# Optimization experiments

Hardware: AMD Instinct MI355X
Metric: run time of the kernel (lower is better)

Reference implementation:

```python
import jax, jax.numpy as jnp
import numpy as np

N = 30000      # num_nodes
R0 = 8         # original relations
R = 2 * R0 + 1 # with inverses + self-loop relation = 17
IN = 256
OUT = 256
E = 300000     # original triples
NB = 8         # num_bases


def setup_inputs() -> dict:
    key = jax.random.key(0)
    k1, k2, k3, k4, k5, k6 = jax.random.split(key, 6)
    s = jax.random.randint(k1, (E,), 0, N)
    r = jax.random.randint(k2, (E,), 0, R0)
    o = jax.random.randint(k3, (E,), 0, N)
    triples = jnp.stack([s, r, o], axis=1)  # [E,3] int
    features = jax.random.normal(k4, (N, IN), dtype=jnp.float32)
    bases = jax.random.normal(k5, (NB, IN, OUT), dtype=jnp.float32) * 0.02
    comps = jax.random.normal(k6, (R, NB), dtype=jnp.float32) * 0.02
    bias = jnp.zeros((OUT,), dtype=jnp.float32)
    return {"triples": triples, "features": features, "bases": bases, "comps": comps, "bias": bias}


def reference(triples, features, bases, comps, bias):
    # basis decomposition: weights[r] = sum_b comps[r,b] * bases[b]
    weights = jnp.einsum('rb,bio->rio', comps, bases)  # [R, IN, OUT]

    s, r, o = triples[:, 0], triples[:, 1], triples[:, 2]
    nodes = jnp.arange(N)
    # eval mode: self_loop_keep_prob = 1 -> all N self loops kept
    src = jnp.concatenate([s, o, nodes])                                  # [E + E + N]
    rel = jnp.concatenate([r, r + R0, jnp.full((N,), 2 * R0, r.dtype)])
    dst = jnp.concatenate([o, s, nodes])

    # horizontal stacking: adj is [N, R*N]; row = src, col = rel*N + dst
    cols = rel * N + dst
    # column normalisation (row_normalisation=False branch of sum_sparse)
    col_sums = jnp.zeros((R * N,), jnp.float32).at[cols].add(1.0)
    sums = col_sums[cols]
    # reorder: swap normalizers of original and inverse edge blocks
    sums = jnp.concatenate([sums[E:2 * E], sums[:E], sums[2 * E:]])
    vals = 1.0 / sums

    # fw[r*N + n] = features[n] @ weights[r]
    fw = jnp.einsum('ni,rio->rno', features, weights).reshape(R * N, OUT)
    msgs = vals[:, None] * fw[cols]                    # [num_edges, OUT]
    out = jnp.zeros((N, OUT), jnp.float32).at[src].add(msgs)
    return out + bias
```

## Files before the change

kernel.cpp:

```cpp
#include <hip/hip_runtime.h>


namespace {
constexpr int kN     = 30000;
constexpr int kR0    = 8;
constexpr int kNRel  = 16;
constexpr int kIN    = 256;
constexpr int kOUT   = 256;
constexpr int kE     = 300000;
constexpr int kNB    = 8;
constexpr int kKT    = kNB * kIN;
constexpr int kRows  = kN * kNRel;
constexpr int kMsgs  = 2 * kE;
constexpr int kScanBlk  = 1024;
constexpr int kNScanBlk = (kRows + kScanBlk - 1) / kScanBlk;
constexpr int kBM    = 128;
constexpr int kMB    = (kN + kBM - 1) / kBM;
constexpr int kMPadAlloc = 30016;
constexpr int kTN    = 16;
}

typedef __bf16 bf16x8 __attribute__((ext_vector_type(8)));
typedef float  f32x4  __attribute__((ext_vector_type(4)));
typedef float  f32x2  __attribute__((ext_vector_type(2)));
typedef float  f32x4v __attribute__((ext_vector_type(4)));
typedef unsigned int u32;

static __device__ __forceinline__ ushort f2bf(float x) {
  unsigned u = __float_as_uint(x);
  u += 0x7FFF + ((u >> 16) & 1);
  return (ushort)(u >> 16);
}

static __device__ __forceinline__ void gload16(const void* g, void* l) {
  __builtin_amdgcn_global_load_lds(
      (const __attribute__((address_space(1))) u32*)g,
      (__attribute__((address_space(3))) u32*)l, 16, 0, 0);
}

#define PKFMA_LO(ACC, G, C) \
  asm("v_pk_fma_f32 %0, %1, %2, %0 op_sel_hi:[1,0,1]" : "+v"(ACC) : "v"(G), "v"(C))
#define PKFMA_HI(ACC, G, C) \
  asm("v_pk_fma_f32 %0, %1, %2, %0 op_sel:[0,1,0] op_sel_hi:[1,1,1]" : "+v"(ACC) : "v"(G), "v"(C))


__global__ void k_prep(const float* __restrict__ f, ushort* __restrict__ fb,
                       const int* __restrict__ t, int* __restrict__ deg,
                       const float* __restrict__ bases, ushort* __restrict__ Bt) {
  int i = blockIdx.x * 256 + threadIdx.x;
  if (i < kN * kIN / 4) {
    float4 v = reinterpret_cast<const float4*>(f)[i];
    ushort4 p;
    p.x = f2bf(v.x); p.y = f2bf(v.y); p.z = f2bf(v.z); p.w = f2bf(v.w);
    reinterpret_cast<ushort4*>(fb)[i] = p;
  }
  if (i < kE) {
    int s = t[3*i], r = t[3*i+1], o = t[3*i+2];
    atomicAdd(&deg[s * kNRel + r], 1);
    atomicAdd(&deg[o * kNRel + kR0 + r], 1);
  }
  if (blockIdx.x < kKT / 16) {
    int b  = blockIdx.x;
    int tt = threadIdx.x;
    char* dst = (char*)Bt + (size_t)tt * 4096;
    int xr = (tt & 7) << 4;
#pragma unroll
    for (int q = 0; q < 4; ++q) {
      int k0 = b * 16 + q * 4;
      ushort4 p;
      p.x = f2bf(bases[(size_t)(k0 + 0) * kOUT + tt]);
      p.y = f2bf(bases[(size_t)(k0 + 1) * kOUT + tt]);
      p.z = f2bf(bases[(size_t)(k0 + 2) * kOUT + tt]);
      p.w = f2bf(bases[(size_t)(k0 + 3) * kOUT + tt]);
      *reinterpret_cast<ushort4*>(dst + ((b * 32 + q * 8) ^ xr)) = p;
    }
  }
}


__global__ void k_scan1(const int* __restrict__ deg, int* __restrict__ rp,
                        int* __restrict__ blksum) {
  __shared__ int s[256];
  int tid = threadIdx.x;
  int base = blockIdx.x * kScanBlk + tid * 4;
  int v0 = 0, v1 = 0, v2 = 0, v3 = 0;
  if (base + 3 < kRows) {
    v0 = deg[base]; v1 = deg[base+1]; v2 = deg[base+2]; v3 = deg[base+3];
  } else {
    if (base     < kRows) v0 = deg[base];
    if (base + 1 < kRows) v1 = deg[base+1];
    if (base + 2 < kRows) v2 = deg[base+2];
  }
  int t0 = v0, t1 = t0 + v1, t2 = t1 + v2, t3 = t2 + v3;
  s[tid] = t3;
  __syncthreads();
  for (int off = 1; off < 256; off <<= 1) {
    int x = 0;
    if (tid >= off) x = s[tid - off];
    __syncthreads();
    s[tid] += x;
    __syncthreads();
  }
  int excl = tid ? s[tid-1] : 0;
  if (base     < kRows) rp[base]   = excl;
  if (base + 1 < kRows) rp[base+1] = excl + t0;
  if (base + 2 < kRows) rp[base+2] = excl + t1;
  if (base + 3 < kRows) rp[base+3] = excl + t2;
  if (tid == 255) blksum[blockIdx.x] = s[255];
}

__global__ void k_scan3(int* __restrict__ rp, const int* __restrict__ blksum) {
  __shared__ int red[256];
  int tid = threadIdx.x;
  int B   = blockIdx.x;
  int region = (B * 256) >> 10;
  int partial = 0;
  for (int k = tid; k < region; k += 256) partial += blksum[k];
  red[tid] = partial;
  __syncthreads();
#pragma unroll
  for (int off = 128; off > 0; off >>= 1) {
    if (tid < off) red[tid] += red[tid + off];
    __syncthreads();
  }
  int base = red[0];
  int i = B * 256 + tid;
  if (i < kRows)       rp[i] += base;
  else if (i == kRows) rp[i]  = kMsgs;
}

__global__ void k_scatter(const int* __restrict__ t, const int* __restrict__ rp,
                          int* __restrict__ deg, int* __restrict__ col) {
  int m = blockIdx.x * 256 + threadIdx.x;
  if (m >= kMsgs) return;
  int e = (m < kE) ? m : m - kE;
  int s = t[3*e], r = t[3*e+1], o = t[3*e+2];
  int rr, tn, sn;
  if (m < kE) { rr = r;        tn = s; sn = o; }
  else        { rr = kR0 + r;  tn = o; sn = s; }
  int idx = tn * kNRel + rr;
  int pos = rp[idx] + (atomicSub(&deg[idx], 1) - 1);
  col[pos] = (rr << 16) | sn;
}

#define FMA4(A, S, G) \
  A.x += (S) * G.x; A.y += (S) * G.y; A.z += (S) * G.z; A.w += (S) * G.w;


__global__ __launch_bounds__(256, 8)
void k_agg1(const int* __restrict__ rp, const int* __restrict__ col,
            const ushort* __restrict__ featbf, const float* __restrict__ comps,
            ushort* __restrict__ aggb) {
  __shared__ float cvb[4][17][kNB];
  int wv   = threadIdx.x >> 6;
  int lane = threadIdx.x & 63;
  int node = blockIdx.x * 4 + wv;

  if (lane < 17) {
    float val = 0.f;
    if (lane < kNRel) {
      int idx = node * kNRel + lane;
      int d = rp[idx + 1] - rp[idx];
      val = d > 0 ? 1.0f / (float)d : 0.f;
    }
#pragma unroll
    for (int b = 0; b < kNB; ++b)
      cvb[wv][lane][b] = comps[lane * kNB + b] * val;
  }
  __syncthreads();

  int se0 = __builtin_amdgcn_readfirstlane(rp[node * kNRel]);
  int se1 = __builtin_amdgcn_readfirstlane(rp[node * kNRel + kNRel]);

  f32x2 accp[2 * kNB];
  {
    uint2 sf = *reinterpret_cast<const uint2*>(featbf + (size_t)node * kIN + lane * 4);
    f32x2 p01, p23;
    p01.x = __uint_as_float(sf.x << 16);
    p01.y = __uint_as_float(sf.x & 0xFFFF0000u);
    p23.x = __uint_as_float(sf.y << 16);
    p23.y = __uint_as_float(sf.y & 0xFFFF0000u);
#pragma unroll
    for (int b = 0; b < kNB; ++b) {
      float cs = comps[2*kR0*kNB + b];
      accp[2*b]     = p01 * cs;
      accp[2*b + 1] = p23 * cs;
    }
  }

  const int pad = (16 << 16);
  int voff = lane * 4;
  const f32x4v* cvr = reinterpret_cast<const f32x4v*>(&cvb[wv][0][0]);

  auto compute = [&](const uint2* g, const int* sc) {
#pragma unroll
    for (int j = 0; j < 4; ++j) {
      int sr = sc[j] >> 16;
      f32x4v cA = cvr[sr * 2];
      f32x4v cB = cvr[sr * 2 + 1];
      f32x2 p01, p23;
      p01.x = __uint_as_float(g[j].x << 16);
      p01.y = __uint_as_float(g[j].x & 0xFFFF0000u);
      p23.x = __uint_as_float(g[j].y << 16);
      p23.y = __uint_as_float(g[j].y & 0xFFFF0000u);
      f32x2 cAl = cA.lo, cAh = cA.hi, cBl = cB.lo, cBh = cB.hi;
      PKFMA_LO(accp[0],  p01, cAl); PKFMA_LO(accp[1],  p23, cAl);
      PKFMA_HI(accp[2],  p01, cAl); PKFMA_HI(accp[3],  p23, cAl);
      PKFMA_LO(accp[4],  p01, cAh); PKFMA_LO(accp[5],  p23, cAh);
      PKFMA_HI(accp[6],  p01, cAh); PKFMA_HI(accp[7],  p23, cAh);
      PKFMA_LO(accp[8],  p01, cBl); PKFMA_LO(accp[9],  p23, cBl);
      PKFMA_HI(accp[10], p01, cBl); PKFMA_HI(accp[11], p23, cBl);
      PKFMA_LO(accp[12], p01, cBh); PKFMA_LO(accp[13], p23, cBh);
      PKFMA_HI(accp[14], p01, cBh); PKFMA_HI(accp[15], p23, cBh);
    }
  };

  int sc0[4], sc1[4];
  uint2 g0[4];
#pragma unroll
  for (int j = 0; j < 4; ++j) {
    int ee = se0 + j;
    int ic = ee < se1 ? ee : 0;
    int v  = col[ic];
    sc0[j] = ee < se1 ? v : pad;
  }
#pragma unroll
  for (int j = 0; j < 4; ++j)
    g0[j] = *reinterpret_cast<const uint2*>(featbf + (size_t)(sc0[j] & 0xFFFF) * kIN + voff);
#pragma unroll
  for (int j = 0; j < 4; ++j) {
    int ee = se0 + 4 + j;
    int ic = ee < se1 ? ee : 0;
    int v  = col[ic];
    sc1[j] = ee < se1 ? v : pad;
  }

  for (int e = se0; e + 4 < se1; e += 4) {
    uint2 g1[4];
#pragma unroll
    for (int j = 0; j < 4; ++j)
      g1[j] = *reinterpret_cast<const uint2*>(featbf + (size_t)(sc1[j] & 0xFFFF) * kIN + voff);
    int sc2[4];
#pragma unroll
    for (int j = 0; j < 4; ++j) {
      int ee = e + 8 + j;
      int ic = ee < se1 ? ee : 0;
      int v  = col[ic];
      sc2[j] = ee < se1 ? v : pad;
    }
    compute(g0, sc0);
#pragma unroll
    for (int j = 0; j < 4; ++j) { g0[j] = g1[j]; sc0[j] = sc1[j]; sc1[j] = sc2[j]; }
  }
  if (se0 < se1) compute(g0, sc0);

  char* rowp = (char*)aggb + (size_t)node * 4096;
  int xr = (node & 7) << 4;
#pragma unroll
  for (int b = 0; b < kNB; ++b) {
    ushort4 p;
    p.x = f2bf(accp[2*b].x);     p.y = f2bf(accp[2*b].y);
    p.z = f2bf(accp[2*b + 1].x); p.w = f2bf(accp[2*b + 1].y);
    *reinterpret_cast<ushort4*>(rowp + ((b * 512 + lane * 8) ^ xr)) = p;
  }
}


__global__ __launch_bounds__(1024, 4)
void k_gemm(const ushort* __restrict__ aggb, const ushort* __restrict__ Bt,
            const float* __restrict__ bias, float* __restrict__ out) {
  __shared__ ushort Albs[2][kBM * 64];
  __shared__ ushort Blds[2][256 * 64];
  int tid  = threadIdx.x;
  int wv   = tid >> 6;
  int lane = tid & 63;
  int mh   = wv >> 2;
  int nq   = wv & 3;
  int l15  = lane & 15;
  int g4   = lane >> 4;
  int node0 = blockIdx.x * kBM;

  f32x4 acc[2][4];
#pragma unroll
  for (int mt = 0; mt < 2; ++mt)
#pragma unroll
    for (int nt = 0; nt < 4; ++nt) acc[mt][nt] = f32x4{0.f, 0.f, 0.f, 0.f};

  auto stage = [&](int c, int buf) {
#pragma unroll
    for (int i = 0; i < 3; ++i) {
      int seg = wv * 3 + i;
      if (seg < 16) {
        int lin = seg * 1024 + lane * 16;
        int row = lin >> 7;
        const char* src = (const char*)aggb + (size_t)(node0 + row) * 4096
                          + c * 128 + (lin & 127);
        gload16(src, (char*)Albs[buf] + seg * 1024);
      } else {
        int t2  = seg - 16;
        int lin = t2 * 1024 + lane * 16;
        int colr = lin >> 7;
        const char* src = (const char*)Bt + (size_t)colr * 4096
                          + c * 128 + (lin & 127);
        gload16(src, (char*)Blds[buf] + t2 * 1024);
      }
    }
  };

  stage(0, 0);
  asm volatile("s_waitcnt vmcnt(0)" ::: "memory");
  __builtin_amdgcn_s_barrier();

  int cur = 0;
  for (int c = 0; c < 32; ++c) {
    if (c + 1 < 32) {
      stage(c + 1, cur ^ 1);
      asm volatile("s_waitcnt vmcnt(3)" ::: "memory");
    } else {
      asm volatile("s_waitcnt vmcnt(0)" ::: "memory");
    }
    __builtin_amdgcn_s_barrier();
    __builtin_amdgcn_sched_barrier(0);
#pragma unroll
    for (int ks = 0; ks < 2; ++ks) {
      int kb = ks * 64 + g4 * 16;
      bf16x8 a[2], b[4];
#pragma unroll
      for (int mt = 0; mt < 2; ++mt) {
        int row = mh * 32 + mt * 16 + l15;
        a[mt] = *reinterpret_cast<const bf16x8*>(
            (const char*)Albs[cur] + row * 128 + (kb ^ ((row & 7) << 4)));
      }
#pragma unroll
      for (int nt = 0; nt < 4; ++nt) {
        int colr = nq * 64 + nt * 16 + l15;
        b[nt] = *reinterpret_cast<const bf16x8*>(
            (const char*)Blds[cur] + colr * 128 + (kb ^ ((colr & 7) << 4)));
      }
#pragma unroll
      for (int mt = 0; mt < 2; ++mt)
#pragma unroll
        for (int nt = 0; nt < 4; ++nt)
          acc[mt][nt] = __builtin_amdgcn_mfma_f32_16x16x32_bf16(a[mt], b[nt],
                                                                acc[mt][nt], 0, 0, 0);
    }
    asm volatile("s_waitcnt lgkmcnt(0)" ::: "memory");
    __builtin_amdgcn_s_barrier();
    cur ^= 1;
  }

#pragma unroll
  for (int nt = 0; nt < 4; ++nt) {
    int colo = nq * 64 + nt * 16 + l15;
    float bi = bias[colo];
#pragma unroll
    for (int mt = 0; mt < 2; ++mt) {
      int rbase = node0 + mh * 32 + mt * 16 + g4 * 4;
#pragma unroll
      for (int j = 0; j < 4; ++j) {
        int row = rbase + j;
        if (row < kN) out[(size_t)row * kOUT + colo] = acc[mt][nt][j] + bi;
      }
    }
  }
}


__global__ __launch_bounds__(512, 4)
void k_out_fused(const int* __restrict__ rp, const int* __restrict__ col,
                 const float* __restrict__ feat, const ushort* __restrict__ featbf,
                 const ushort* __restrict__ Bt, const float* __restrict__ comps,
                 const float* __restrict__ bias, float* __restrict__ out) {
  __shared__ ushort aggs[kTN * kKT];
  __shared__ float  cvb[kTN][17][kNB];
  int tid  = threadIdx.x;
  int wv   = tid >> 6;
  int lane = tid & 63;
  int node0 = blockIdx.x * kTN;

  for (int q = tid; q < kTN * 17; q += 512) {
    int nl = q / 17, rl = q - nl * 17;
    float val = 0.f;
    if (rl < kNRel) {
      int idx = (node0 + nl) * kNRel + rl;
      int d = rp[idx + 1] - rp[idx];
      val = d > 0 ? 1.0f / (float)d : 0.f;
    }
#pragma unroll
    for (int b = 0; b < kNB; ++b)
      cvb[nl][rl][b] = comps[rl * kNB + b] * val;
  }
  __syncthreads();

  for (int half = 0; half < 2; ++half) {
    int nl   = (wv << 1) | half;
    int node = node0 + nl;
    int e0 = rp[node * kNRel];
    int e1 = rp[node * kNRel + kNRel];

    float4 f = *reinterpret_cast<const float4*>(feat + (size_t)node * kIN + lane * 4);
    float4 acc[kNB];
#pragma unroll
    for (int b = 0; b < kNB; ++b) {
      float cs = comps[2*kR0*kNB + b];
      acc[b].x = cs * f.x; acc[b].y = cs * f.y; acc[b].z = cs * f.z; acc[b].w = cs * f.w;
    }
    const float4* cvr = reinterpret_cast<const float4*>(&cvb[nl][0][0]);
    const int pad = (16 << 16);
    int cc[4];
#pragma unroll
    for (int j = 0; j < 4; ++j) {
      int ee = e0 + j;
      int v  = col[ee < kMsgs ? ee : kMsgs - 1];
      cc[j] = ee < e1 ? v : pad;
    }
    for (int e = e0; e < e1; e += 4) {
      uint2 g[4];
#pragma unroll
      for (int j = 0; j < 4; ++j) {
        int sn = cc[j] & 0xFFFF;
        g[j] = *reinterpret_cast<const uint2*>(featbf + (size_t)sn * kIN + lane * 4);
      }
      int rr[4];
#pragma unroll
      for (int j = 0; j < 4; ++j) rr[j] = cc[j] >> 16;
#pragma unroll
      for (int j = 0; j < 4; ++j) {
        int ee = e + 4 + j;
        int v  = col[ee < kMsgs ? ee : kMsgs - 1];
        cc[j] = ee < e1 ? v : pad;
      }
#pragma unroll
      for (int j = 0; j < 4; ++j) {
        float4 c0 = cvr[rr[j] * 2];
        float4 c1 = cvr[rr[j] * 2 + 1];
        float4 gg;
        gg.x = __uint_as_float(g[j].x << 16);
        gg.y = __uint_as_float(g[j].x & 0xFFFF0000u);
        gg.z = __uint_as_float(g[j].y << 16);
        gg.w = __uint_as_float(g[j].y & 0xFFFF0000u);
        FMA4(acc[0], c0.x, gg) FMA4(acc[1], c0.y, gg)
        FMA4(acc[2], c0.z, gg) FMA4(acc[3], c0.w, gg)
        FMA4(acc[4], c1.x, gg) FMA4(acc[5], c1.y, gg)
        FMA4(acc[6], c1.z, gg) FMA4(acc[7], c1.w, gg)
      }
    }
    int xr = (nl & 7) << 4;
#pragma unroll
    for (int b = 0; b < kNB; ++b) {
      ushort4 p;
      p.x = f2bf(acc[b].x); p.y = f2bf(acc[b].y);
      p.z = f2bf(acc[b].z); p.w = f2bf(acc[b].w);
      int byteoff = nl * 4096 + ((b * 512 + lane * 8) ^ xr);
      *reinterpret_cast<ushort4*>(reinterpret_cast<char*>(aggs) + byteoff) = p;
    }
  }
  __syncthreads();

  {
    int n  = lane & 15;
    int g4 = lane >> 4;
    const char* abase = reinterpret_cast<const char*>(aggs) + n * 4096;
    int axor = (n & 7) << 4;
#pragma unroll
    for (int t = 0; t < 2; ++t) {
      int ntile = wv + t * 8;
      float bi = bias[ntile * 16 + n];
      const char* btrow = reinterpret_cast<const char*>(Bt)
                          + (size_t)(ntile * 16 + n) * 4096;
      int bxor = (n & 7) << 4;
      f32x4 acc = {0.f, 0.f, 0.f, 0.f};
#pragma unroll 4
      for (int ks = 0; ks < kKT / 32; ++ks) {
        int kb = ks * 64 + g4 * 16;
        bf16x8 af = *reinterpret_cast<const bf16x8*>(abase + (kb ^ axor));
        bf16x8 bf = *reinterpret_cast<const bf16x8*>(btrow + (kb ^ bxor));
        acc = __builtin_amdgcn_mfma_f32_16x16x32_bf16(af, bf, acc, 0, 0, 0);
      }
#pragma unroll
      for (int j = 0; j < 4; ++j) {
        int row = g4 * 4 + j;
        out[(size_t)(node0 + row) * kOUT + ntile * 16 + n] = acc[j] + bi;
      }
    }
  }
}


extern "C" void kernel_launch(void* const* d_in, const int* in_sizes, int n_in,
                              void* d_out, int out_size, void* d_ws, size_t ws_size,
                              hipStream_t stream) {
  const int*   triples = (const int*)  d_in[0];
  const float* feat    = (const float*)d_in[1];
  const float* bases   = (const float*)d_in[2];
  const float* comps   = (const float*)d_in[3];
  const float* bias    = (const float*)d_in[4];
  float* out = (float*)d_out;

  size_t featbf_b = (size_t)kN * kIN * 2;
  size_t bt_b     = (size_t)kOUT * kKT * 2;
  size_t aggb_b   = (size_t)kMPadAlloc * kKT * 2;
  size_t csr_b    = (size_t)(kRows + kRows + 1 + kMsgs + kNScanBlk) * 4;
  bool bigws = ws_size >= featbf_b + bt_b + aggb_b + csr_b + 1024;

  char* p = (char*)d_ws;
  ushort* featbf = (ushort*)p;            p += featbf_b;
  ushort* Bt     = (ushort*)p;            p += bt_b;
  ushort* aggb   = nullptr;
  if (bigws) { aggb = (ushort*)p;         p += aggb_b; }
  int* deg    = (int*)p;
  int* rp     = deg + kRows;
  int* col    = rp + kRows + 1;
  int* blksum = col + kMsgs;

  hipMemsetAsync(deg, 0, kRows * sizeof(int), stream);
  k_prep  <<<(kN * kIN / 4 + 255) / 256, 256, 0, stream>>>(feat, featbf, triples, deg,
                                                           bases, Bt);
  k_scan1 <<<kNScanBlk,             256, 0, stream>>>(deg, rp, blksum);
  k_scan3 <<<(kRows + 256) / 256,   256, 0, stream>>>(rp, blksum);
  k_scatter<<<(kMsgs + 255) / 256,  256, 0, stream>>>(triples, rp, deg, col);

  if (bigws) {
    k_agg1<<<kN / 4,   256, 0, stream>>>(rp, col, featbf, comps, aggb);
    k_gemm<<<kMB,     1024, 0, stream>>>(aggb, Bt, bias, out);
  } else {
    k_out_fused<<<kN / kTN, 512, 0, stream>>>(rp, col, feat, featbf, Bt,
                                              comps, bias, out);
  }
}
```

Measured before the change: 177.1 us.

## Shrink GEMM tile to 64 rows with 256-thread blocks, drop double buffering

The aggregated-feature GEMM now uses 64-row M tiles with 4 waves per block. Each wave covers all 64 rows and one 64-column slice, so it holds a 4x4 grid of accumulator tiles. The LDS double buffer and the prefetch of the next K chunk are removed, and each chunk is now loaded, waited on and computed in sequence. The aim is more blocks (better CU fill across 30000 rows) and less LDS per block for higher occupancy. The cost is that load latency is no longer overlapped within a block, and the B matrix is re-fetched by twice as many blocks.

```diff
diff --git a/kernel.cpp b/kernel.cpp
--- a/kernel.cpp
+++ b/kernel.cpp
@@ -14,7 +14,7 @@
 constexpr int kMsgs  = 2 * kE;
 constexpr int kScanBlk  = 1024;
 constexpr int kNScanBlk = (kRows + kScanBlk - 1) / kScanBlk;
-constexpr int kBM    = 128;
+constexpr int kBM    = 64;
 constexpr int kMB    = (kN + kBM - 1) / kBM;
 constexpr int kMPadAlloc = 30016;
 constexpr int kTN    = 16;
@@ -266,79 +266,64 @@
 }
 
 
-__global__ __launch_bounds__(1024, 4)
+__global__ __launch_bounds__(256, 4)
 void k_gemm(const ushort* __restrict__ aggb, const ushort* __restrict__ Bt,
             const float* __restrict__ bias, float* __restrict__ out) {
-  __shared__ ushort Albs[2][kBM * 64];
-  __shared__ ushort Blds[2][256 * 64];
+  __shared__ ushort Albs[kBM * 64];
+  __shared__ ushort Blds[256 * 64];
   int tid  = threadIdx.x;
   int wv   = tid >> 6;
   int lane = tid & 63;
-  int mh   = wv >> 2;
-  int nq   = wv & 3;
   int l15  = lane & 15;
   int g4   = lane >> 4;
   int node0 = blockIdx.x * kBM;
 
-  f32x4 acc[2][4];
-#pragma unroll
-  for (int mt = 0; mt < 2; ++mt)
+  f32x4 acc[4][4];
+#pragma unroll
+  for (int mt = 0; mt < 4; ++mt)
 #pragma unroll
     for (int nt = 0; nt < 4; ++nt) acc[mt][nt] = f32x4{0.f, 0.f, 0.f, 0.f};
 
-  auto stage = [&](int c, int buf) {
-#pragma unroll
-    for (int i = 0; i < 3; ++i) {
-      int seg = wv * 3 + i;
-      if (seg < 16) {
+  for (int c = 0; c < 32; ++c) {
+#pragma unroll
+    for (int i = 0; i < 10; ++i) {
+      int seg = wv * 10 + i;
+      if (seg < 8) {
         int lin = seg * 1024 + lane * 16;
         int row = lin >> 7;
         const char* src = (const char*)aggb + (size_t)(node0 + row) * 4096
                           + c * 128 + (lin & 127);
-        gload16(src, (char*)Albs[buf] + seg * 1024);
+        gload16(src, (char*)Albs + seg * 1024);
       } else {
-        int t2  = seg - 16;
-        int lin = t2 * 1024 + lane * 16;
+        int s2  = seg - 8;
+        int lin = s2 * 1024 + lane * 16;
         int colr = lin >> 7;
         const char* src = (const char*)Bt + (size_t)colr * 4096
                           + c * 128 + (lin & 127);
-        gload16(src, (char*)Blds[buf] + t2 * 1024);
-      }
-    }
-  };
-
-  stage(0, 0);
-  asm volatile("s_waitcnt vmcnt(0)" ::: "memory");
-  __builtin_amdgcn_s_barrier();
-
-  int cur = 0;
-  for (int c = 0; c < 32; ++c) {
-    if (c + 1 < 32) {
-      stage(c + 1, cur ^ 1);
-      asm volatile("s_waitcnt vmcnt(3)" ::: "memory");
-    } else {
-      asm volatile("s_waitcnt vmcnt(0)" ::: "memory");
-    }
+        gload16(src, (char*)Blds + s2 * 1024);
+      }
+    }
+    asm volatile("s_waitcnt vmcnt(0)" ::: "memory");
     __builtin_amdgcn_s_barrier();
-    __builtin_amdgcn_sched_barrier(0);
+
 #pragma unroll
     for (int ks = 0; ks < 2; ++ks) {
       int kb = ks * 64 + g4 * 16;
-      bf16x8 a[2], b[4];
-#pragma unroll
-      for (int mt = 0; mt < 2; ++mt) {
-        int row = mh * 32 + mt * 16 + l15;
+      bf16x8 a[4], b[4];
+#pragma unroll
+      for (int mt = 0; mt < 4; ++mt) {
+        int row = mt * 16 + l15;
         a[mt] = *reinterpret_cast<const bf16x8*>(
-            (const char*)Albs[cur] + row * 128 + (kb ^ ((row & 7) << 4)));
+            (const char*)Albs + row * 128 + (kb ^ ((row & 7) << 4)));
       }
 #pragma unroll
       for (int nt = 0; nt < 4; ++nt) {
-        int colr = nq * 64 + nt * 16 + l15;
+        int colr = wv * 64 + nt * 16 + l15;
         b[nt] = *reinterpret_cast<const bf16x8*>(
-            (const char*)Blds[cur] + colr * 128 + (kb ^ ((colr & 7) << 4)));
-      }
-#pragma unroll
-      for (int mt = 0; mt < 2; ++mt)
+            (const char*)Blds + colr * 128 + (kb ^ ((colr & 7) << 4)));
+      }
+#pragma unroll
+      for (int mt = 0; mt < 4; ++mt)
 #pragma unroll
         for (int nt = 0; nt < 4; ++nt)
           acc[mt][nt] = __builtin_amdgcn_mfma_f32_16x16x32_bf16(a[mt], b[nt],
@@ -346,16 +331,15 @@
     }
     asm volatile("s_waitcnt lgkmcnt(0)" ::: "memory");
     __builtin_amdgcn_s_barrier();
-    cur ^= 1;
   }
 
 #pragma unroll
   for (int nt = 0; nt < 4; ++nt) {
-    int colo = nq * 64 + nt * 16 + l15;
+    int colo = wv * 64 + nt * 16 + l15;
     float bi = bias[colo];
 #pragma unroll
-    for (int mt = 0; mt < 2; ++mt) {
-      int rbase = node0 + mh * 32 + mt * 16 + g4 * 4;
+    for (int mt = 0; mt < 4; ++mt) {
+      int rbase = node0 + mt * 16 + g4 * 4;
 #pragma unroll
       for (int j = 0; j < 4; ++j) {
         int row = rbase + j;
@@ -521,8 +505,8 @@
   k_scatter<<<(kMsgs + 255) / 256,  256, 0, stream>>>(triples, rp, deg, col);
 
   if (bigws) {
-    k_agg1<<<kN / 4,   256, 0, stream>>>(rp, col, featbf, comps, aggb);
-    k_gemm<<<kMB,     1024, 0, stream>>>(aggb, Bt, bias, out);
+    k_agg1<<<kN / 4, 256, 0, stream>>>(rp, col, featbf, comps, aggb);
+    k_gemm<<<kMB,    256, 0, stream>>>(aggb, Bt, bias, out);
   } else {
     k_out_fused<<<kN / kTN, 512, 0, stream>>>(rp, col, feat, featbf, Bt,
                                               comps, bias, out);
```

New measurement: 241.9 us. +36.6%, slower.
